# Kernel optimization log

Measured on AMD Instinct MI355X. Metric: run time of the kernel, lower is better.

The kernel has to match this reference:

```python
import jax, jax.numpy as jnp
import numpy as np

CODEBOOK_SIZE = 1024
NUM_GROUPS = 8
CODES_PER_GROUP = CODEBOOK_SIZE // NUM_GROUPS
COMMITMENT_COST = 0.25


def setup_inputs() -> dict:
    key = jax.random.key(0)
    k1, k2, k3 = jax.random.split(key, 3)
    B, C, H, W = 32, 256, 32, 32
    z = jax.random.normal(k1, (B, C, H, W), dtype=jnp.float32)
    # matches nn.Embedding init: uniform(-1/n_e, 1/n_e)
    emb_weight = jax.random.uniform(
        k2, (CODEBOOK_SIZE, C), dtype=jnp.float32,
        minval=-1.0 / CODEBOOK_SIZE, maxval=1.0 / CODEBOOK_SIZE)
    # proj initialized near identity (nn.init.eye_), perturbed so it is non-trivial
    proj_weight = jnp.eye(C, dtype=jnp.float32) + 0.01 * jax.random.normal(
        k3, (C, C), dtype=jnp.float32)
    return {"z": z, "emb_weight": emb_weight, "proj_weight": proj_weight}


def reference(z, emb_weight, proj_weight):
    # z: [B, C, H, W] -> [B, H, W, C]
    B, C, H, W = z.shape
    zc = jnp.transpose(z, (0, 2, 3, 1))          # bhwc
    zf = zc.reshape(-1, C)                        # [N, C], N = B*H*W

    # codebook = embedding_proj(embedding.weight) = emb @ proj.T
    codebook = emb_weight @ proj_weight.T         # [n_e, C]

    # squared L2 distances: [N, n_e]
    d = (jnp.sum(zf * zf, axis=1, keepdims=True)
         + jnp.sum(codebook * codebook, axis=1)
         - 2.0 * (zf @ codebook.T))

    # group-restricted mask: token group depends on width position
    pos_groups = (jnp.arange(W) * NUM_GROUPS) // W          # [W]
    token_groups = jnp.tile(pos_groups, B * H)              # [N]
    code_groups = jnp.arange(CODEBOOK_SIZE) // CODES_PER_GROUP  # [n_e]
    valid = token_groups[:, None] == code_groups[None, :]   # [N, n_e]
    d = jnp.where(valid, d, jnp.inf)

    idx = jnp.argmin(d, axis=1)                   # [N]
    zq = codebook[idx].reshape(zc.shape)          # [B, H, W, C]

    commitment_loss = COMMITMENT_COST * jnp.mean(
        (jax.lax.stop_gradient(zq) - zc) ** 2)
    codebook_loss = jnp.mean((zq - jax.lax.stop_gradient(zc)) ** 2)
    loss = commitment_loss + codebook_loss

    # straight-through estimator
    zq_ste = zc + jax.lax.stop_gradient(zq - zc)
    zq_out = jnp.transpose(zq_ste, (0, 3, 1, 2))  # [B, C, H, W]

    return (zq_out, loss, commitment_loss, codebook_loss,
            idx.reshape(B, H, W))
```

## Files before the change

### kernel.cpp

```cpp
#include <hip/hip_runtime.h>

#define CODEBOOK 1024
#define NGROUPS  8
#define CPG      128
#define Bn 32
#define Cn 256
#define Hn 32
#define Wn 32

#define ZQ_OFF   0
#define LOSS_OFF (Bn*Cn*Hn*Wn)
#define IDX_OFF  (LOSS_OFF + 3)

__global__ __launch_bounds__(256) void transpose_proj(const float* __restrict__ proj,
                                                      float* __restrict__ projT) {
    int k = blockIdx.x;
    int j = threadIdx.x;
    projT[(size_t)k * Cn + j] = proj[(size_t)j * Cn + k];
}

__global__ __launch_bounds__(256) void codebook_kernel(const float* __restrict__ emb,
                                                       const float* __restrict__ projT,
                                                       float* __restrict__ cb) {
    __shared__ float emb8[8][Cn];
    const int t  = threadIdx.x;
    const int i0 = blockIdx.x * 8;
#pragma unroll
    for (int m = 0; m < 8; ++m) {
        int id = t + m * 256;
        int ci = id >> 8, k = id & 255;
        emb8[ci][k] = emb[(size_t)(i0 + ci) * Cn + k];
    }
    __syncthreads();
    float acc[8] = {0.f,0.f,0.f,0.f,0.f,0.f,0.f,0.f};
    for (int k = 0; k < Cn; ++k) {
        float pj = projT[(size_t)k * Cn + t];
#pragma unroll
        for (int ci = 0; ci < 8; ++ci)
            acc[ci] = __builtin_fmaf(emb8[ci][k], pj, acc[ci]);
    }
#pragma unroll
    for (int ci = 0; ci < 8; ++ci)
        cb[(size_t)(i0 + ci) * Cn + t] = acc[ci];
}

__global__ __launch_bounds__(64) void norm_kernel(const float* __restrict__ cb,
                                                  float* __restrict__ norms) {
    int i = blockIdx.x, l = threadIdx.x;
    float4 v = *(const float4*)(cb + (size_t)i * Cn + l * 4);
    float s = v.x*v.x + v.y*v.y + v.z*v.z + v.w*v.w;
#pragma unroll
    for (int off = 32; off > 0; off >>= 1) s += __shfl_down(s, off);
    if (l == 0) norms[i] = s;
}

__global__ __launch_bounds__(256) void vq_main(const float* __restrict__ z,
                                               const float* __restrict__ cb,
                                               const float* __restrict__ norms,
                                               float* __restrict__ out,
                                               double* __restrict__ lacc) {
    __shared__ float ztile[64][64];
    __shared__ float cbt[128][64];
    __shared__ float zfin[64];
    __shared__ float red_d[64][16];
    __shared__ int   red_c[64][16];
    __shared__ int   bestidx[64];

    const int t   = threadIdx.x;
    const int bid = blockIdx.x;
    const int g   = bid & 7;
    const int ht  = (bid >> 3) & 1;
    const int b   = bid >> 4;
    const int h0  = ht * 16;
    const int w0  = g * 4;

    const float* zb  = z  + (size_t)b * (Cn * Hn * Wn);
    const float* cbg = cb + (size_t)g * CPG * Cn;

    const int tok0  = (t & 15) * 4;
    const int code0 = (t >> 4) * 8;

    float acc[4][8];
#pragma unroll
    for (int r = 0; r < 4; ++r)
#pragma unroll
        for (int c = 0; c < 8; ++c) acc[r][c] = 0.f;

    float zr[16];
#pragma unroll
    for (int q = 0; q < 16; ++q) zr[q] = 0.f;

    for (int kc = 0; kc < 4; ++kc) {
        const int k0 = kc * 64;
#pragma unroll
        for (int m = 0; m < 4; ++m) {
            int id = t + m * 256;
            int kk = id >> 4, i = id & 15;
            float4 v = *(const float4*)(zb + (size_t)(k0 + kk) * (Hn * Wn)
                                        + (h0 + i) * Wn + w0);
            *(float4*)&ztile[kk][i * 4] = v;
        }
#pragma unroll
        for (int m = 0; m < 8; ++m) {
            int id = t + m * 256;
            int ci = id >> 4, kq = id & 15;
            float4 v = *(const float4*)(cbg + (size_t)ci * Cn + k0 + kq * 4);
            *(float4*)&cbt[ci][kq * 4] = v;
        }
        __syncthreads();

        if (t < 64) {
#pragma clang fp contract(off)
            {
                const int base8 = (kc >> 1) * 8;
                for (int kk = 0; kk < 64; ++kk) {
                    float v  = ztile[kk][t];
                    float sq = v * v;
                    zr[base8 + (kk & 7)] += sq;
                }
            }
        }

        for (int kb = 0; kb < 16; ++kb) {
            const int kk = kb * 4;
            float4 zt[4];
#pragma unroll
            for (int u = 0; u < 4; ++u)
                zt[u] = *(const float4*)&ztile[kk + u][tok0];
            float4 cf[8];
#pragma unroll
            for (int c = 0; c < 8; ++c)
                cf[c] = *(const float4*)&cbt[code0 + c][kk];
#pragma unroll
            for (int u = 0; u < 4; ++u) {
                const float zu[4] = {
                    zt[u].x, zt[u].y, zt[u].z, zt[u].w };
                const float cu[8] = {
                    ((const float*)&cf[0])[u], ((const float*)&cf[1])[u],
                    ((const float*)&cf[2])[u], ((const float*)&cf[3])[u],
                    ((const float*)&cf[4])[u], ((const float*)&cf[5])[u],
                    ((const float*)&cf[6])[u], ((const float*)&cf[7])[u] };
#pragma unroll
                for (int r = 0; r < 4; ++r)
#pragma unroll
                    for (int c = 0; c < 8; ++c)
                        acc[r][c] = __builtin_fmaf(zu[r], cu[c], acc[r][c]);
            }
        }
        __syncthreads();
    }

    if (t < 64) {
#pragma clang fp contract(off)
        {
            float zh0 = ((zr[0] + zr[1]) + (zr[2] + zr[3]))
                      + ((zr[4] + zr[5]) + (zr[6] + zr[7]));
            float zh1 = ((zr[8] + zr[9]) + (zr[10] + zr[11]))
                      + ((zr[12] + zr[13]) + (zr[14] + zr[15]));
            zfin[t] = zh0 + zh1;
        }
    }
    __syncthreads();

    float nv[8];
    *(float4*)&nv[0] = *(const float4*)(norms + g * CPG + code0);
    *(float4*)&nv[4] = *(const float4*)(norms + g * CPG + code0 + 4);
#pragma unroll
    for (int r = 0; r < 4; ++r) {
        float zv = zfin[tok0 + r];
        float bd = __builtin_inff();
        int   bc = 0;
#pragma unroll
        for (int c = 0; c < 8; ++c) {
            float s = zv + nv[c];
            float d = s - 2.0f * acc[r][c];
            if (d < bd) { bd = d; bc = code0 + c; }
        }
        red_d[tok0 + r][t >> 4] = bd;
        red_c[tok0 + r][t >> 4] = bc;
    }
    __syncthreads();

    if (t < 64) {
        float bd = red_d[t][0];
        int   bc = red_c[t][0];
        for (int q = 1; q < 16; ++q) {
            float d = red_d[t][q];
            if (d < bd) { bd = d; bc = red_c[t][q]; }
        }
        int gidx = g * CPG + bc;
        bestidx[t] = gidx;
        int h = h0 + (t >> 2), w = w0 + (t & 3);
        out[IDX_OFF + b * (Hn * Wn) + h * Wn + w] = (float)gidx;
    }
    __syncthreads();

    float lsum = 0.f;
    const size_t zbase = (size_t)b * (Cn * Hn * Wn);
#pragma unroll
    for (int m = 0; m < 16; ++m) {
        int id = t + m * 256;
        int c = id >> 4, i = id & 15;
        size_t off = zbase + (size_t)c * (Hn * Wn) + (h0 + i) * Wn + w0;
        float4 zv = *(const float4*)(z + off);
        float q0 = cb[(size_t)bestidx[i * 4 + 0] * Cn + c];
        float q1 = cb[(size_t)bestidx[i * 4 + 1] * Cn + c];
        float q2 = cb[(size_t)bestidx[i * 4 + 2] * Cn + c];
        float q3 = cb[(size_t)bestidx[i * 4 + 3] * Cn + c];
        float4 o; o.x = q0; o.y = q1; o.z = q2; o.w = q3;
        *(float4*)(out + ZQ_OFF + off) = o;
        float d0 = q0 - zv.x, d1 = q1 - zv.y, d2 = q2 - zv.z, d3 = q3 - zv.w;
        lsum = __builtin_fmaf(d0, d0, lsum);
        lsum = __builtin_fmaf(d1, d1, lsum);
        lsum = __builtin_fmaf(d2, d2, lsum);
        lsum = __builtin_fmaf(d3, d3, lsum);
    }
    __syncthreads();
    float* rr = &red_d[0][0];
    rr[t] = lsum;
    __syncthreads();
    for (int s2 = 128; s2 > 0; s2 >>= 1) {
        if (t < s2) rr[t] += rr[t + s2];
        __syncthreads();
    }
    if (t == 0) atomicAdd(lacc, (double)rr[0]);
}

__global__ void finalize(const double* __restrict__ lacc, float* __restrict__ out) {
    float M    = (float)(lacc[0] / (double)(Bn * Cn * Hn * Wn));
    float comm = 0.25f * M;
    out[LOSS_OFF + 0] = comm + M;
    out[LOSS_OFF + 1] = comm;
    out[LOSS_OFF + 2] = M;
}

extern "C" void kernel_launch(void* const* d_in, const int* in_sizes, int n_in,
                              void* d_out, int out_size, void* d_ws, size_t ws_size,
                              hipStream_t stream) {
    (void)in_sizes; (void)n_in; (void)out_size; (void)ws_size;
    const float* z    = (const float*)d_in[0];
    const float* emb  = (const float*)d_in[1];
    const float* proj = (const float*)d_in[2];
    float* out = (float*)d_out;

    char*   ws    = (char*)d_ws;
    float*  projT = (float*)ws;
    float*  cb    = (float*)(ws + 262144);
    float*  norms = (float*)(ws + 262144 + 1048576);
    double* lacc  = (double*)(ws + 262144 + 1048576 + 4096);

    hipMemsetAsync(lacc, 0, sizeof(double), stream);
    transpose_proj <<<Cn,        256, 0, stream>>>(proj, projT);
    codebook_kernel<<<CODEBOOK/8,256, 0, stream>>>(emb, projT, cb);
    norm_kernel    <<<CODEBOOK,   64, 0, stream>>>(cb, norms);
    vq_main        <<<Bn*2*NGROUPS,256,0, stream>>>(z, cb, norms, out, lacc);
    finalize       <<<1, 1, 0, stream>>>(lacc, out);
}
```

Measured before the change: 212.5 us.

## Swizzle codebook tile in LDS, remap block order, fold memset into kernel

The codebook tile in shared memory is now stored with an XOR swizzle on its float4 column index, so the per-thread reads of 8 consecutive code rows land in different LDS banks instead of conflicting. Block indices are remapped so that consecutive blocks share the same codebook group, which aims to improve L2 reuse of each group's codebook slice across CUs/XCDs. The hipMemsetAsync of the loss accumulator is replaced by a store inside the first kernel, removing one launch. Several loop variables are renamed to avoid shadowing the new block-mapping variables.

```diff
diff --git a/kernel.cpp b/kernel.cpp
--- a/kernel.cpp
+++ b/kernel.cpp
@@ -13,7 +13,9 @@
 #define IDX_OFF  (LOSS_OFF + 3)
 
 __global__ __launch_bounds__(256) void transpose_proj(const float* __restrict__ proj,
-                                                      float* __restrict__ projT) {
+                                                      float* __restrict__ projT,
+                                                      double* __restrict__ lacc) {
+    if (blockIdx.x == 0 && threadIdx.x == 0) lacc[0] = 0.0;
     int k = blockIdx.x;
     int j = threadIdx.x;
     projT[(size_t)k * Cn + j] = proj[(size_t)j * Cn + k];
@@ -68,9 +70,12 @@
 
     const int t   = threadIdx.x;
     const int bid = blockIdx.x;
-    const int g   = bid & 7;
-    const int ht  = (bid >> 3) & 1;
-    const int b   = bid >> 4;
+    const int r   = bid & 7;
+    const int q   = bid >> 3;
+    const int g   = q & 7;
+    const int s   = ((q >> 3) << 3) | r;
+    const int ht  = s & 1;
+    const int b   = s >> 1;
     const int h0  = ht * 16;
     const int w0  = g * 4;
 
@@ -82,13 +87,13 @@
 
     float acc[4][8];
 #pragma unroll
-    for (int r = 0; r < 4; ++r)
-#pragma unroll
-        for (int c = 0; c < 8; ++c) acc[r][c] = 0.f;
+    for (int rr2 = 0; rr2 < 4; ++rr2)
+#pragma unroll
+        for (int c = 0; c < 8; ++c) acc[rr2][c] = 0.f;
 
     float zr[16];
 #pragma unroll
-    for (int q = 0; q < 16; ++q) zr[q] = 0.f;
+    for (int p = 0; p < 16; ++p) zr[p] = 0.f;
 
     for (int kc = 0; kc < 4; ++kc) {
         const int k0 = kc * 64;
@@ -105,7 +110,7 @@
             int id = t + m * 256;
             int ci = id >> 4, kq = id & 15;
             float4 v = *(const float4*)(cbg + (size_t)ci * Cn + k0 + kq * 4);
-            *(float4*)&cbt[ci][kq * 4] = v;
+            ((float4*)&cbt[ci][0])[kq ^ (ci >> 3)] = v;
         }
         __syncthreads();
 
@@ -130,7 +135,7 @@
             float4 cf[8];
 #pragma unroll
             for (int c = 0; c < 8; ++c)
-                cf[c] = *(const float4*)&cbt[code0 + c][kk];
+                cf[c] = ((const float4*)&cbt[code0 + c][0])[kb ^ ((code0 + c) >> 3)];
 #pragma unroll
             for (int u = 0; u < 4; ++u) {
                 const float zu[4] = {
@@ -141,10 +146,10 @@
                     ((const float*)&cf[4])[u], ((const float*)&cf[5])[u],
                     ((const float*)&cf[6])[u], ((const float*)&cf[7])[u] };
 #pragma unroll
-                for (int r = 0; r < 4; ++r)
+                for (int rr3 = 0; rr3 < 4; ++rr3)
 #pragma unroll
                     for (int c = 0; c < 8; ++c)
-                        acc[r][c] = __builtin_fmaf(zu[r], cu[c], acc[r][c]);
+                        acc[rr3][c] = __builtin_fmaf(zu[rr3], cu[c], acc[rr3][c]);
             }
         }
         __syncthreads();
@@ -166,27 +171,27 @@
     *(float4*)&nv[0] = *(const float4*)(norms + g * CPG + code0);
     *(float4*)&nv[4] = *(const float4*)(norms + g * CPG + code0 + 4);
 #pragma unroll
-    for (int r = 0; r < 4; ++r) {
-        float zv = zfin[tok0 + r];
+    for (int rr4 = 0; rr4 < 4; ++rr4) {
+        float zv = zfin[tok0 + rr4];
         float bd = __builtin_inff();
         int   bc = 0;
 #pragma unroll
         for (int c = 0; c < 8; ++c) {
-            float s = zv + nv[c];
-            float d = s - 2.0f * acc[r][c];
+            float ss = zv + nv[c];
+            float d  = ss - 2.0f * acc[rr4][c];
             if (d < bd) { bd = d; bc = code0 + c; }
         }
-        red_d[tok0 + r][t >> 4] = bd;
-        red_c[tok0 + r][t >> 4] = bc;
+        red_d[tok0 + rr4][t >> 4] = bd;
+        red_c[tok0 + rr4][t >> 4] = bc;
     }
     __syncthreads();
 
     if (t < 64) {
         float bd = red_d[t][0];
         int   bc = red_c[t][0];
-        for (int q = 1; q < 16; ++q) {
-            float d = red_d[t][q];
-            if (d < bd) { bd = d; bc = red_c[t][q]; }
+        for (int p = 1; p < 16; ++p) {
+            float d = red_d[t][p];
+            if (d < bd) { bd = d; bc = red_c[t][p]; }
         }
         int gidx = g * CPG + bc;
         bestidx[t] = gidx;
@@ -249,8 +254,7 @@
     float*  norms = (float*)(ws + 262144 + 1048576);
     double* lacc  = (double*)(ws + 262144 + 1048576 + 4096);
 
-    hipMemsetAsync(lacc, 0, sizeof(double), stream);
-    transpose_proj <<<Cn,        256, 0, stream>>>(proj, projT);
+    transpose_proj <<<Cn,        256, 0, stream>>>(proj, projT, lacc);
     codebook_kernel<<<CODEBOOK/8,256, 0, stream>>>(emb, projT, cb);
     norm_kernel    <<<CODEBOOK,   64, 0, stream>>>(cb, norms);
     vq_main        <<<Bn*2*NGROUPS,256,0, stream>>>(z, cb, norms, out, lacc);
```

New measurement: 175.7 us. -17.3%, faster.
